# Performance work log

Measured on AMD Instinct MI355X. Metric: run time of the kernel, lower is better.

The kernel has to match this reference:

```python
import jax, jax.numpy as jnp
import numpy as np

DIM, E, K = 256, 8, 2
B, D, H, W = 1, 32, 32, 32
EPS = 1e-5


def setup_inputs() -> dict:
    key = jax.random.key(0)
    ks = jax.random.split(key, 16)
    nrm = lambda k, s, sc=0.02: jax.random.normal(k, s, jnp.float32) * sc
    def resblock_params(k):
        k1, k2, k3, k4 = jax.random.split(k, 4)
        return dict(
            c1w=nrm(k1, (DIM, DIM, 3, 3, 3)), c1b=jnp.zeros((DIM,), jnp.float32),
            g1=jax.random.uniform(k2, (DIM,), jnp.float32, 0.5, 1.5), be1=jnp.zeros((DIM,), jnp.float32),
            c2w=nrm(k3, (DIM, DIM, 3, 3, 3)), c2b=jnp.zeros((DIM,), jnp.float32),
            g2=jax.random.uniform(k4, (DIM,), jnp.float32, 0.5, 1.5), be2=jnp.zeros((DIM,), jnp.float32),
        )
    p1 = resblock_params(ks[5])
    p2 = resblock_params(ks[6])
    return {
        "x": jax.random.normal(ks[0], (B, DIM, D, H, W), jnp.float32),
        "wg": nrm(ks[1], (DIM, E)),
        "w1": nrm(ks[2], (E, DIM, DIM)), "b1": jnp.zeros((E, DIM), jnp.float32),
        "w2": nrm(ks[3], (E, DIM, DIM)), "b2": jnp.zeros((E, DIM), jnp.float32),
        "r1_c1w": p1["c1w"], "r1_c1b": p1["c1b"], "r1_g1": p1["g1"], "r1_be1": p1["be1"],
        "r1_c2w": p1["c2w"], "r1_c2b": p1["c2b"], "r1_g2": p1["g2"], "r1_be2": p1["be2"],
        "r2_c1w": p2["c1w"], "r2_c1b": p2["c1b"], "r2_g1": p2["g1"], "r2_be1": p2["be1"],
        "r2_c2w": p2["c2w"], "r2_c2b": p2["c2b"], "r2_g2": p2["g2"], "r2_be2": p2["be2"],
        "c8w": nrm(ks[4], (DIM, DIM, 1, 1, 1)), "c8b": jnp.zeros((DIM,), jnp.float32),
    }


def conv3d(x, w, b, pad):
    y = jax.lax.conv_general_dilated(
        x, w, window_strides=(1, 1, 1), padding=[(pad, pad)] * 3,
        dimension_numbers=("NCDHW", "OIDHW", "NCDHW"))
    return y + b[None, :, None, None, None]


def batchnorm(x, g, b):
    m = x.mean(axis=(0, 2, 3, 4), keepdims=True)
    v = x.var(axis=(0, 2, 3, 4), keepdims=True)
    return g[None, :, None, None, None] * (x - m) * jax.lax.rsqrt(v + EPS) + b[None, :, None, None, None]


def unet_res_block(x, c1w, c1b, g1, be1, c2w, c2b, g2, be2):
    out = jax.nn.leaky_relu(batchnorm(conv3d(x, c1w, c1b, 1), g1, be1), 0.01)
    out = batchnorm(conv3d(out, c2w, c2b, 1), g2, be2)
    return jax.nn.leaky_relu(out + x, 0.01)  # identity shortcut (in==out ch, stride 1)


def mom_block(x, wg, w1, b1, w2, b2):
    Bb, C, Dd, Hh, Ww = x.shape
    tokens = x.transpose(0, 2, 3, 4, 1).reshape(-1, C)  # [T, C]
    T = tokens.shape[0]
    probs = jax.nn.softmax(tokens @ wg, axis=-1)          # [T, E]
    vals, idx = jax.lax.top_k(probs, K)                   # [T, K]
    wts = vals / vals.sum(-1, keepdims=True)
    gates = jnp.zeros((T, E), probs.dtype).at[jnp.arange(T)[:, None], idx].set(wts)
    # dense expert MLPs (math-equivalent to gather/dispatch/combine)
    h = jax.nn.gelu(jnp.einsum("tc,ech->eth", tokens, w1) + b1[:, None, :])
    eo = jnp.einsum("eth,ehc->etc", h, w2) + b2[:, None, :]
    moe = jnp.einsum("te,etc->tc", gates, eo)             # [T, C]
    # switch-style load-balancing auxiliary loss
    density = (gates > 0).astype(probs.dtype).mean(0)     # fraction of tokens per expert
    density_proxy = probs.mean(0)
    aux = (density * density_proxy).sum() * E
    out = x + moe.reshape(Bb, Dd, Hh, Ww, C).transpose(0, 4, 1, 2, 3)
    return out, aux


def reference(x, wg, w1, b1, w2, b2,
              r1_c1w, r1_c1b, r1_g1, r1_be1, r1_c2w, r1_c2b, r1_g2, r1_be2,
              r2_c1w, r2_c1b, r2_g1, r2_be1, r2_c2w, r2_c2b, r2_g2, r2_be2,
              c8w, c8b):
    xm, aux = mom_block(x, wg, w1, b1, w2, b2)
    res = unet_res_block(xm, r1_c1w, r1_c1b, r1_g1, r1_be1, r1_c2w, r1_c2b, r1_g2, r1_be2)
    res = unet_res_block(res, r2_c1w, r2_c1b, r2_g1, r2_be1, r2_c2w, r2_c2b, r2_g2, r2_be2)
    out = xm + conv3d(res, c8w, c8b, 0)  # Dropout3d is identity at eval
    return out, aux
```

## Files before the change

kernel.cpp:

```cpp
#include <hip/hip_runtime.h>
#include <stdint.h>

typedef __attribute__((ext_vector_type(8))) short short8;
typedef __attribute__((ext_vector_type(4))) float f32x4;
typedef unsigned short u16;
typedef unsigned int u32;
typedef unsigned long long u64;

#define WS_TOK   0ull
#define WS_XT    16777216ull
#define WS_XMCT  50331648ull
#define WS_GATES 83886080ull
#define WS_PART  84934656ull
#define WS_MOE   101711872ull
#define WS_P1    135266304ull
#define WS_P2    155389952ull
#define WS_Y     175513600ull
#define WS_R2    209068032ull
#define WS_WRB   225845248ull
#define WS_W1P   240001024ull
#define WS_W2P   241049600ull
#define WS_C8P   242098176ull
#define WS_SF    242753536ull
#define WS_AUXP  242755584ull

__device__ __forceinline__ u16 f2bf(float f) {
  u32 x = __float_as_uint(f);
  u32 r = x + 0x7fffu + ((x >> 16) & 1u);
  return (u16)(r >> 16);
}

__global__ void trans_in_k(const float* __restrict__ x, float* __restrict__ xt,
                           u16* __restrict__ tok) {
  __shared__ float ld[64][65];
  int tt = blockIdx.x, cc = blockIdx.y, tid = threadIdx.x;
#pragma unroll
  for (int k = 0; k < 16; ++k) {
    int idx = tid + k * 256;
    int cl = idx >> 6, j = idx & 63;
    ld[cl][j] = x[(size_t)(cc * 64 + cl) * 32768 + tt * 64 + j];
  }
  __syncthreads();
#pragma unroll
  for (int k = 0; k < 16; ++k) {
    int idx = tid + k * 256;
    int tl = idx >> 6, cl = idx & 63;
    float v = ld[cl][tl];
    size_t o = (size_t)(tt * 64 + tl) * 256 + cc * 64 + cl;
    xt[o] = v;
    tok[o] = f2bf(v);
  }
}

__global__ void pack_rb_k(const float* __restrict__ w0, const float* __restrict__ w1,
                          const float* __restrict__ w2, const float* __restrict__ w3,
                          u16* __restrict__ out) {
  __shared__ float ld[6912];
  int conv = blockIdx.x >> 8, blk = blockIdx.x & 255, tid = threadIdx.x;
  const float* src = conv == 0 ? w0 : conv == 1 ? w1 : conv == 2 ? w2 : w3;
  size_t base = (size_t)blk * 256 * 27;
#pragma unroll
  for (int k = 0; k < 27; ++k) ld[tid + k * 256] = src[base + tid + k * 256];
  __syncthreads();
  u16* dst = out + (size_t)conv * 27 * 65536;
  int n = blk * 256 + tid;
#pragma unroll
  for (int tap = 0; tap < 27; ++tap)
    dst[(size_t)tap * 65536 + n] = f2bf(ld[tid * 27 + tap]);
}

__global__ void pack_tr_k(const float* __restrict__ w1, const float* __restrict__ w2,
                          u16* __restrict__ w1p, u16* __restrict__ w2p) {
  __shared__ float ld[64][65];
  int m = blockIdx.y, tile = blockIdx.x, tid = threadIdx.x;
  const float* src = (m < 8) ? (w1 + (size_t)m * 65536) : (w2 + (size_t)(m - 8) * 65536);
  u16* dst = (m < 8) ? (w1p + (size_t)m * 65536) : (w2p + (size_t)(m - 8) * 65536);
  int r0 = (tile >> 2) * 64, c0 = (tile & 3) * 64;
#pragma unroll
  for (int k = 0; k < 16; ++k) {
    int idx = tid + k * 256;
    int rr = idx >> 6, cc = idx & 63;
    ld[rr][cc] = src[(size_t)(r0 + rr) * 256 + c0 + cc];
  }
  __syncthreads();
#pragma unroll
  for (int k = 0; k < 16; ++k) {
    int idx = tid + k * 256;
    int cc = idx >> 6, rr = idx & 63;
    dst[(size_t)(c0 + cc) * 256 + r0 + rr] = f2bf(ld[rr][cc]);
  }
}

__global__ void cvt_k(const float* __restrict__ in, u16* __restrict__ out, int n) {
  int i = blockIdx.x * 256 + threadIdx.x;
  if (i < n) out[i] = f2bf(in[i]);
}

__global__ void halo_k(u16* __restrict__ P1, u16* __restrict__ P2) {
  int gid = blockIdx.x * 256 + threadIdx.x;
  int r = gid >> 5, o = (gid & 31) << 3;
  if (r >= 39304) return;
  int d = r / 1156, rem = r - d * 1156, h = rem / 34, w = rem - h * 34;
  if (d >= 1 && d <= 32 && h >= 1 && h <= 32 && w >= 1 && w <= 32) return;
  uint4 z = {0u, 0u, 0u, 0u};
  *(uint4*)(P1 + (size_t)r * 256 + o) = z;
  *(uint4*)(P2 + (size_t)r * 256 + o) = z;
}

__global__ void gate_k(const float* __restrict__ xt, const float* __restrict__ wg,
                       float* __restrict__ gates, float* __restrict__ auxp) {
  __shared__ float wgs[2048];
  __shared__ float ax[4][16];
  int tid = threadIdx.x;
#pragma unroll
  for (int k = 0; k < 8; ++k) wgs[tid + k * 256] = wg[tid + k * 256];
  __syncthreads();
  int t = blockIdx.x * 256 + tid;
  int lane = tid & 63, wv = tid >> 6;
  float l[8] = {0, 0, 0, 0, 0, 0, 0, 0};
  const float* xr = xt + (size_t)t * 256;
  for (int c = 0; c < 256; c += 4) {
    float4 xv = *(const float4*)(xr + c);
#pragma unroll
    for (int e = 0; e < 8; ++e)
      l[e] += xv.x * wgs[c * 8 + e] + xv.y * wgs[(c + 1) * 8 + e] +
              xv.z * wgs[(c + 2) * 8 + e] + xv.w * wgs[(c + 3) * 8 + e];
  }
  float mx = l[0];
#pragma unroll
  for (int e = 1; e < 8; ++e) mx = fmaxf(mx, l[e]);
  float p[8], sum = 0.f;
#pragma unroll
  for (int e = 0; e < 8; ++e) { p[e] = __expf(l[e] - mx); sum += p[e]; }
  float inv = 1.0f / sum;
#pragma unroll
  for (int e = 0; e < 8; ++e) p[e] *= inv;
  int i0 = 0; float v0 = p[0];
#pragma unroll
  for (int e = 1; e < 8; ++e) if (p[e] > v0) { v0 = p[e]; i0 = e; }
  int i1 = -1; float v1 = -1.0f;
#pragma unroll
  for (int e = 0; e < 8; ++e) if (e != i0 && p[e] > v1) { v1 = p[e]; i1 = e; }
  float wsum = v0 + v1;
  float g0 = v0 / wsum, g1 = v1 / wsum;
  float* gr = gates + (size_t)t * 8;
#pragma unroll
  for (int e = 0; e < 8; ++e) gr[e] = (e == i0) ? g0 : (e == i1) ? g1 : 0.0f;
#pragma unroll
  for (int e = 0; e < 8; ++e) {
    float ps = p[e];
    float cn = (e == i0 || e == i1) ? 1.0f : 0.0f;
    for (int o = 32; o; o >>= 1) { ps += __shfl_down(ps, o); cn += __shfl_down(cn, o); }
    if (lane == 0) { ax[wv][e] = ps; ax[wv][8 + e] = cn; }
  }
  __syncthreads();
  if (tid < 16)
    auxp[blockIdx.x * 16 + tid] = ax[0][tid] + ax[1][tid] + ax[2][tid] + ax[3][tid];
}

__global__ void aux_k(const float* __restrict__ auxp, float* __restrict__ out) {
  __shared__ float s[16];
  int i = threadIdx.x;
  if (i < 16) {
    float a = 0;
    for (int b = 0; b < 128; ++b) a += auxp[b * 16 + i];
    s[i] = a;
  }
  __syncthreads();
  if (i == 0) {
    float r = 0;
    for (int e = 0; e < 8; ++e)
      r += (s[8 + e] * (1.0f / 32768.0f)) * (s[e] * (1.0f / 32768.0f));
    out[0] = r * 8.0f;
  }
}

__global__ __launch_bounds__(512, 2) void moe_k(
    const u16* __restrict__ tok, const u16* __restrict__ w1p,
    const u16* __restrict__ w2p, const float* __restrict__ b1,
    const float* __restrict__ b2, const float* __restrict__ gates,
    float* __restrict__ moe) {
  __shared__ __attribute__((aligned(16))) unsigned char smem[163840];
  const int tid = threadIdx.x;
  const int ttile = blockIdx.x;
  const int lane = tid & 63;
  const int wv = tid >> 6;
  const int wr = (wv >> 2) * 64;
  const int wc = (wv & 3) * 64;
  const int fq = lane >> 4, fr = lane & 15;

#pragma unroll
  for (int it = 0; it < 8; ++it) {
    int s = tid + it * 512;
    int r = s >> 5, seg = s & 31;
    int cole = ((seg >> 3) << 6) + (((seg & 7) ^ (r & 7)) << 3);
    __builtin_amdgcn_global_load_lds(
        (const __attribute__((address_space(1))) u32*)(tok + (size_t)(ttile * 128 + r) * 256 + cole),
        (__attribute__((address_space(3))) u32*)(smem + s * 16), 16, 0, 0);
  }

  f32x4 macc[4][4];
#pragma unroll
  for (int m = 0; m < 4; ++m)
#pragma unroll
    for (int n = 0; n < 4; ++n) macc[m][n] = (f32x4){0.f, 0.f, 0.f, 0.f};

#pragma unroll 1
  for (int e = 0; e < 8; ++e) {
    const u16* w1e = w1p + e * 65536;
    const u16* w2e = w2p + e * 65536;

    f32x4 acc1[4][4];
#pragma unroll
    for (int mc = 0; mc < 4; ++mc)
#pragma unroll
      for (int nt = 0; nt < 4; ++nt) acc1[mc][nt] = (f32x4){0.f, 0.f, 0.f, 0.f};

#pragma unroll 1
    for (int kc = 0; kc < 4; ++kc) {
#pragma unroll
      for (int it = 0; it < 4; ++it) {
        int s = tid + it * 512;
        int r = s >> 3;
        int sub = (s & 7) ^ (r & 7);
        __builtin_amdgcn_global_load_lds(
            (const __attribute__((address_space(1))) u32*)(w1e + (size_t)r * 256 + kc * 64 + sub * 8),
            (__attribute__((address_space(3))) u32*)(smem + 65536 + s * 16), 16, 0, 0);
      }
      __syncthreads();
#pragma unroll
      for (int khf = 0; khf < 2; ++khf) {
        short8 af1[4], bt[4];
#pragma unroll
        for (int mc = 0; mc < 4; ++mc) {
          int row = wc + mc * 16 + fr;
          int p = (khf * 4 + fq) ^ (row & 7);
          af1[mc] = *(const short8*)(smem + 65536 + row * 128 + p * 16);
        }
#pragma unroll
        for (int nt = 0; nt < 4; ++nt) {
          int row = wr + nt * 16 + fr;
          int p = (khf * 4 + fq) ^ (row & 7);
          bt[nt] = *(const short8*)(smem + row * 512 + kc * 128 + p * 16);
        }
#pragma unroll
        for (int mc = 0; mc < 4; ++mc)
#pragma unroll
          for (int nt = 0; nt < 4; ++nt)
            acc1[mc][nt] = __builtin_amdgcn_mfma_f32_16x16x32_bf16(af1[mc], bt[nt], acc1[mc][nt], 0, 0, 0);
      }
      __syncthreads();
    }

#pragma unroll
    for (int mc = 0; mc < 4; ++mc) {
      int k0 = wc + mc * 16 + fq * 4;
      float4 bv = *(const float4*)(b1 + e * 256 + k0);
#pragma unroll
      for (int nt = 0; nt < 4; ++nt) {
        int t = wr + nt * 16 + fr;
        u64 pk = 0;
#pragma unroll
        for (int j = 0; j < 4; ++j) {
          float v = acc1[mc][nt][j] + ((const float*)&bv)[j];
          float u = 1.5957691216057308f * (v + 0.044715f * v * v * v);
          float g = v / (1.0f + __expf(-u));
          pk |= (u64)f2bf(g) << (16 * j);
        }
        *(u64*)(smem + 98304 + t * 512 + ((k0 * 2) ^ ((t & 7) << 4))) = pk;
      }
    }

    f32x4 acc2[4][4];
#pragma unroll
    for (int m = 0; m < 4; ++m)
#pragma unroll
      for (int n = 0; n < 4; ++n) acc2[m][n] = (f32x4){0.f, 0.f, 0.f, 0.f};

#pragma unroll 1
    for (int kc = 0; kc < 4; ++kc) {
#pragma unroll
      for (int it = 0; it < 4; ++it) {
        int s = tid + it * 512;
        int r = s >> 3;
        int sub = (s & 7) ^ (r & 7);
        __builtin_amdgcn_global_load_lds(
            (const __attribute__((address_space(1))) u32*)(w2e + (size_t)r * 256 + kc * 64 + sub * 8),
            (__attribute__((address_space(3))) u32*)(smem + 65536 + s * 16), 16, 0, 0);
      }
      __syncthreads();
#pragma unroll
      for (int khf = 0; khf < 2; ++khf) {
        short8 af[4], bb[4];
#pragma unroll
        for (int m = 0; m < 4; ++m) {
          int row = wr + m * 16 + fr;
          int col = (kc * 128 + (khf * 4 + fq) * 16) ^ ((row & 7) << 4);
          af[m] = *(const short8*)(smem + 98304 + row * 512 + col);
        }
#pragma unroll
        for (int n = 0; n < 4; ++n) {
          int row = wc + n * 16 + fr;
          int p = (khf * 4 + fq) ^ (row & 7);
          bb[n] = *(const short8*)(smem + 65536 + row * 128 + p * 16);
        }
#pragma unroll
        for (int m = 0; m < 4; ++m)
#pragma unroll
          for (int n = 0; n < 4; ++n)
            acc2[m][n] = __builtin_amdgcn_mfma_f32_16x16x32_bf16(af[m], bb[n], acc2[m][n], 0, 0, 0);
      }
      __syncthreads();
    }

    float bs2[4];
#pragma unroll
    for (int n = 0; n < 4; ++n) bs2[n] = b2[e * 256 + wc + n * 16 + fr];
#pragma unroll
    for (int m = 0; m < 4; ++m)
#pragma unroll
      for (int j = 0; j < 4; ++j) {
        int t = ttile * 128 + wr + m * 16 + fq * 4 + j;
        float g = gates[(size_t)t * 8 + e];
#pragma unroll
        for (int n = 0; n < 4; ++n)
          macc[m][n][j] += g * (acc2[m][n][j] + bs2[n]);
      }
  }

#pragma unroll
  for (int m = 0; m < 4; ++m)
#pragma unroll
    for (int j = 0; j < 4; ++j) {
      int t = ttile * 128 + wr + m * 16 + fq * 4 + j;
      float* mr = moe + (size_t)t * 256 + wc;
#pragma unroll
      for (int n = 0; n < 4; ++n) mr[n * 16 + fr] = macc[m][n][j];
    }
}

template <int MODE>
__global__ __launch_bounds__(256, 2) void gemm_k(
    const u16* __restrict__ A, const u16* __restrict__ Bw,
    const float* __restrict__ bias, float* __restrict__ outF,
    const float* __restrict__ xmct, float* __restrict__ part) {
  __shared__ __attribute__((aligned(16))) unsigned char smem[32768];
  const int tid = threadIdx.x;
  const int ttile = blockIdx.x;
  const int ctile = blockIdx.y;
  const int lane = tid & 63;
  const int wv = tid >> 6;
  const int wr = (wv >> 1) << 6;
  const int wc = (wv & 1) << 6;
  const int fq = lane >> 4;
  const int fr = lane & 15;

  int aoff[4], boff[4];
#pragma unroll
  for (int it = 0; it < 4; ++it) {
    int s = tid + it * 256;
    int r = s >> 3;
    int lsg = (s & 7) ^ (r & 7);
    if (MODE == 0) {
      int dd = ttile >> 3;
      int h0 = (ttile & 7) << 2;
      int base = dd * 1156 + (h0 + (r >> 5)) * 34 + (r & 31);
      aoff[it] = base * 256 + lsg * 8;
    } else {
      aoff[it] = (ttile * 128 + r) * 256 + lsg * 8;
    }
    boff[it] = (ctile * 128 + r) * 256 + lsg * 8;
  }

  f32x4 acc[4][4];
#pragma unroll
  for (int m = 0; m < 4; ++m)
#pragma unroll
    for (int n = 0; n < 4; ++n) acc[m][n] = (f32x4){0.f, 0.f, 0.f, 0.f};

  const int nTap = (MODE == 0) ? 27 : 1;
#pragma unroll 1
  for (int tap = 0; tap < nTap; ++tap) {
    int atap = 0, btap = 0;
    if (MODE == 0) {
      atap = ((tap / 9) * 1156 + ((tap / 3) % 3) * 34 + (tap % 3)) * 256;
      btap = tap * 65536;
    }
#pragma unroll 1
    for (int kc = 0; kc < 4; ++kc) {
      const u16* Ak = A + atap + kc * 64;
      const u16* Bk = Bw + btap + kc * 64;
#pragma unroll
      for (int it = 0; it < 4; ++it) {
        __builtin_amdgcn_global_load_lds(
            (const __attribute__((address_space(1))) u32*)(Ak + aoff[it]),
            (__attribute__((address_space(3))) u32*)(smem + (tid + it * 256) * 16),
            16, 0, 0);
        __builtin_amdgcn_global_load_lds(
            (const __attribute__((address_space(1))) u32*)(Bk + boff[it]),
            (__attribute__((address_space(3))) u32*)(smem + 16384 + (tid + it * 256) * 16),
            16, 0, 0);
      }
      __syncthreads();
#pragma unroll
      for (int khf = 0; khf < 2; ++khf) {
        short8 af[4], bb[4];
#pragma unroll
        for (int m = 0; m < 4; ++m) {
          int row = wr + m * 16 + fr;
          int p = (khf * 4 + fq) ^ (row & 7);
          af[m] = *(const short8*)(smem + row * 128 + p * 16);
        }
#pragma unroll
        for (int n = 0; n < 4; ++n) {
          int row = wc + n * 16 + fr;
          int p = (khf * 4 + fq) ^ (row & 7);
          bb[n] = *(const short8*)(smem + 16384 + row * 128 + p * 16);
        }
#pragma unroll
        for (int m = 0; m < 4; ++m)
#pragma unroll
          for (int n = 0; n < 4; ++n)
            acc[m][n] = __builtin_amdgcn_mfma_f32_16x16x32_bf16(af[m], bb[n], acc[m][n], 0, 0, 0);
      }
      __syncthreads();
    }
  }

  float bs[4];
#pragma unroll
  for (int n = 0; n < 4; ++n) bs[n] = bias[ctile * 128 + wc + n * 16 + fr];

  if (MODE == 3) {
#pragma unroll
    for (int m = 0; m < 4; ++m) {
      int trow = ttile * 128 + wr + m * 16 + fq * 4;
#pragma unroll
      for (int n = 0; n < 4; ++n) {
        int oc = ctile * 128 + wc + n * 16 + fr;
        size_t o = (size_t)oc * 32768 + trow;
        float4 xv = *(const float4*)(xmct + o);
        float4 w;
        w.x = acc[m][n][0] + bs[n] + xv.x;
        w.y = acc[m][n][1] + bs[n] + xv.y;
        w.z = acc[m][n][2] + bs[n] + xv.z;
        w.w = acc[m][n][3] + bs[n] + xv.w;
        *(float4*)(outF + o) = w;
      }
    }
  } else {
    float sn[4] = {0, 0, 0, 0}, qn[4] = {0, 0, 0, 0};
#pragma unroll
    for (int m = 0; m < 4; ++m) {
#pragma unroll
      for (int j = 0; j < 4; ++j) {
        int t = ttile * 128 + wr + m * 16 + fq * 4 + j;
        float* yr = outF + (size_t)t * 256 + ctile * 128 + wc;
#pragma unroll
        for (int n = 0; n < 4; ++n) {
          float v = acc[m][n][j] + bs[n];
          yr[n * 16 + fr] = v;
          sn[n] += v;
          qn[n] += v * v;
        }
      }
    }
#pragma unroll
    for (int n = 0; n < 4; ++n) {
      float s = sn[n], q = qn[n];
      s += __shfl_xor(s, 16); s += __shfl_xor(s, 32);
      q += __shfl_xor(q, 16); q += __shfl_xor(q, 32);
      if (lane < 16) {
        int pi = (ttile * 2 + (wv >> 1)) * 256 + ctile * 128 + wc + n * 16 + fr;
        part[pi] = s;
        part[131072 + pi] = q;
      }
    }
  }
}

__global__ void stats2_k(const float* __restrict__ part, const float* __restrict__ g,
                         const float* __restrict__ be, float* __restrict__ sf) {
  __shared__ float sred[4][256], qred[4][256];
  int tid = threadIdx.x;
  int c = tid & 255, qd = tid >> 8;
  float s = 0, q = 0;
  for (int b = qd * 128; b < qd * 128 + 128; ++b) {
    s += part[b * 256 + c];
    q += part[131072 + b * 256 + c];
  }
  sred[qd][c] = s;
  qred[qd][c] = q;
  __syncthreads();
  if (qd == 0) {
    s = sred[0][c] + sred[1][c] + sred[2][c] + sred[3][c];
    q = qred[0][c] + qred[1][c] + qred[2][c] + qred[3][c];
    float mean = s * (1.0f / 32768.0f);
    float var = q * (1.0f / 32768.0f) - mean * mean;
    float a = g[c] * rsqrtf(var + 1e-5f);
    sf[c] = a;
    sf[256 + c] = be[c] - mean * a;
  }
}

template <int V>
__global__ void bn_k(const float* __restrict__ y, const float* __restrict__ sf,
                     const float* __restrict__ skip, u16* __restrict__ pad,
                     float* __restrict__ f32o, u16* __restrict__ bfo) {
  int gid = blockIdx.x * 256 + threadIdx.x;
  int t = gid >> 5, c0 = (gid & 31) << 3;
  size_t base = (size_t)t * 256 + c0;
  float v[8];
  const float4* yp = (const float4*)(y + base);
  float4 y0 = yp[0], y1 = yp[1];
  const float4* ap = (const float4*)(sf + c0);
  float4 a0 = ap[0], a1 = ap[1];
  const float4* shp = (const float4*)(sf + 256 + c0);
  float4 s0 = shp[0], s1 = shp[1];
  v[0] = a0.x * y0.x + s0.x; v[1] = a0.y * y0.y + s0.y;
  v[2] = a0.z * y0.z + s0.z; v[3] = a0.w * y0.w + s0.w;
  v[4] = a1.x * y1.x + s1.x; v[5] = a1.y * y1.y + s1.y;
  v[6] = a1.z * y1.z + s1.z; v[7] = a1.w * y1.w + s1.w;
  if (V >= 1) {
    const float4* kp = (const float4*)(skip + base);
    float4 k0 = kp[0], k1 = kp[1];
    v[0] += k0.x; v[1] += k0.y; v[2] += k0.z; v[3] += k0.w;
    v[4] += k1.x; v[5] += k1.y; v[6] += k1.z; v[7] += k1.w;
  }
#pragma unroll
  for (int i = 0; i < 8; ++i) v[i] = v[i] > 0.0f ? v[i] : 0.01f * v[i];
  if (V <= 1) {
    int d = t >> 10, h = (t >> 5) & 31, w = t & 31;
    int prow = (d + 1) * 1156 + (h + 1) * 34 + (w + 1);
    uint4 pk;
    pk.x = (u32)f2bf(v[0]) | ((u32)f2bf(v[1]) << 16);
    pk.y = (u32)f2bf(v[2]) | ((u32)f2bf(v[3]) << 16);
    pk.z = (u32)f2bf(v[4]) | ((u32)f2bf(v[5]) << 16);
    pk.w = (u32)f2bf(v[6]) | ((u32)f2bf(v[7]) << 16);
    *(uint4*)(pad + (size_t)prow * 256 + c0) = pk;
  }
  if (V == 1) {
    float4 o0 = {v[0], v[1], v[2], v[3]}, o1 = {v[4], v[5], v[6], v[7]};
    float4* fp = (float4*)(f32o + base);
    fp[0] = o0; fp[1] = o1;
  }
  if (V == 2) {
    uint4 pk;
    pk.x = (u32)f2bf(v[0]) | ((u32)f2bf(v[1]) << 16);
    pk.y = (u32)f2bf(v[2]) | ((u32)f2bf(v[3]) << 16);
    pk.z = (u32)f2bf(v[4]) | ((u32)f2bf(v[5]) << 16);
    pk.w = (u32)f2bf(v[6]) | ((u32)f2bf(v[7]) << 16);
    *(uint4*)(bfo + base) = pk;
  }
}

__global__ void xm_k(float* __restrict__ xt, const float* __restrict__ moe,
                     float* __restrict__ xmct, u16* __restrict__ pad) {
  __shared__ float ld[64][65];
  int tt = blockIdx.x, cc = blockIdx.y, tid = threadIdx.x;
#pragma unroll
  for (int k = 0; k < 16; ++k) {
    int idx = tid + k * 256;
    int tl = idx >> 6, cl = idx & 63;
    size_t o = (size_t)(tt * 64 + tl) * 256 + cc * 64 + cl;
    float v = xt[o] + moe[o];
    xt[o] = v;
    ld[tl][cl] = v;
    int t = tt * 64 + tl;
    int d = t >> 10, h = (t >> 5) & 31, w = t & 31;
    int prow = (d + 1) * 1156 + (h + 1) * 34 + (w + 1);
    pad[(size_t)prow * 256 + cc * 64 + cl] = f2bf(v);
  }
  __syncthreads();
#pragma unroll
  for (int k = 0; k < 16; ++k) {
    int idx = tid + k * 256;
    int cl = idx >> 6, tl = idx & 63;
    xmct[(size_t)(cc * 64 + cl) * 32768 + tt * 64 + tl] = ld[tl][cl];
  }
}

extern "C" void kernel_launch(void* const* d_in, const int* in_sizes, int n_in,
                              void* d_out, int out_size, void* d_ws, size_t ws_size,
                              hipStream_t stream) {
  (void)in_sizes; (void)n_in; (void)out_size; (void)ws_size;
  const float* x  = (const float*)d_in[0];
  const float* wg = (const float*)d_in[1];
  const float* w1 = (const float*)d_in[2];
  const float* b1 = (const float*)d_in[3];
  const float* w2 = (const float*)d_in[4];
  const float* b2 = (const float*)d_in[5];

  char* ws = (char*)d_ws;
  u16* tok    = (u16*)(ws + WS_TOK);
  float* xt   = (float*)(ws + WS_XT);
  float* xmct = (float*)(ws + WS_XMCT);
  float* gates= (float*)(ws + WS_GATES);
  float* part = (float*)(ws + WS_PART);
  float* moe  = (float*)(ws + WS_MOE);
  u16* P1     = (u16*)(ws + WS_P1);
  u16* P2     = (u16*)(ws + WS_P2);
  float* ybuf = (float*)(ws + WS_Y);
  u16* r2b    = (u16*)(ws + WS_R2);
  u16* wrb    = (u16*)(ws + WS_WRB);
  u16* w1p    = (u16*)(ws + WS_W1P);
  u16* w2p    = (u16*)(ws + WS_W2P);
  u16* c8p    = (u16*)(ws + WS_C8P);
  float* sf   = (float*)(ws + WS_SF);
  float* auxp = (float*)(ws + WS_AUXP);
  float* outp = (float*)d_out;

  halo_k<<<4913, 256, 0, stream>>>(P1, P2);
  trans_in_k<<<dim3(512, 4), 256, 0, stream>>>(x, xt, tok);
  pack_rb_k<<<1024, 256, 0, stream>>>((const float*)d_in[6], (const float*)d_in[10],
                                      (const float*)d_in[14], (const float*)d_in[18], wrb);
  pack_tr_k<<<dim3(16, 16), 256, 0, stream>>>(w1, w2, w1p, w2p);
  cvt_k<<<256, 256, 0, stream>>>((const float*)d_in[22], c8p, 65536);
  gate_k<<<128, 256, 0, stream>>>(xt, wg, gates, auxp);

  moe_k<<<256, 512, 0, stream>>>(tok, w1p, w2p, b1, b2, gates, moe);
  xm_k<<<dim3(512, 4), 256, 0, stream>>>(xt, moe, xmct, P1);

  gemm_k<0><<<dim3(256, 2), 256, 0, stream>>>(P1, wrb + 0 * 1769472, (const float*)d_in[7],
                                              ybuf, nullptr, part);
  stats2_k<<<1, 1024, 0, stream>>>(part, (const float*)d_in[8], (const float*)d_in[9], sf);
  bn_k<0><<<4096, 256, 0, stream>>>(ybuf, sf, nullptr, P2, nullptr, nullptr);
  gemm_k<0><<<dim3(256, 2), 256, 0, stream>>>(P2, wrb + 1 * 1769472, (const float*)d_in[11],
                                              ybuf, nullptr, part);
  stats2_k<<<1, 1024, 0, stream>>>(part, (const float*)d_in[12], (const float*)d_in[13], sf);
  bn_k<1><<<4096, 256, 0, stream>>>(ybuf, sf, xt, P1, xt, nullptr);

  gemm_k<0><<<dim3(256, 2), 256, 0, stream>>>(P1, wrb + 2 * 1769472, (const float*)d_in[15],
                                              ybuf, nullptr, part);
  stats2_k<<<1, 1024, 0, stream>>>(part, (const float*)d_in[16], (const float*)d_in[17], sf);
  bn_k<0><<<4096, 256, 0, stream>>>(ybuf, sf, nullptr, P2, nullptr, nullptr);
  gemm_k<0><<<dim3(256, 2), 256, 0, stream>>>(P2, wrb + 3 * 1769472, (const float*)d_in[19],
                                              ybuf, nullptr, part);
  stats2_k<<<1, 1024, 0, stream>>>(part, (const float*)d_in[20], (const float*)d_in[21], sf);
  bn_k<2><<<4096, 256, 0, stream>>>(ybuf, sf, xt, nullptr, nullptr, r2b);

  gemm_k<3><<<dim3(256, 2), 256, 0, stream>>>(r2b, c8p, (const float*)d_in[23], outp,
                                              xmct, nullptr);
  aux_k<<<1, 64, 0, stream>>>(auxp, outp + 8388608);
}
```

Before: 778.2 us.

## Replace dense MoE over all experts with sparse top-2 token dispatch

Instead of running every token through all 8 expert MLPs and weighting by gates, the gate kernel now records top-2 selections and per-block counts. A scan and scatter then build a per-expert permutation padded to 128-row tiles. A grouped GEMM kernel processes only routed tokens per expert tile and writes bf16 outputs, and a combine kernel gathers the two expert outputs per token. This cuts expert FLOPs roughly fourfold, at the cost of extra small launches, gathered loads and a bf16 rounding of expert outputs. The conv GEMM tile order is also swizzled for mode 0.

Result: faster. 718.3 us (-7.7%).

```diff
diff --git a/kernel.cpp b/kernel.cpp
--- a/kernel.cpp
+++ b/kernel.cpp
@@ -11,7 +11,7 @@
 #define WS_XT    16777216ull
 #define WS_XMCT  50331648ull
 #define WS_GATES 83886080ull
-#define WS_PART  84934656ull
+#define WS_H     84934656ull
 #define WS_MOE   101711872ull
 #define WS_P1    135266304ull
 #define WS_P2    155389952ull
@@ -21,8 +21,16 @@
 #define WS_W1P   240001024ull
 #define WS_W2P   241049600ull
 #define WS_C8P   242098176ull
-#define WS_SF    242753536ull
-#define WS_AUXP  242755584ull
+#define WS_PART  242229248ull
+#define WS_SF    243277824ull
+#define WS_AUXP  243279872ull
+
+#define WS_PERM  (WS_H + 0x00000ull)
+#define WS_TBL   (WS_H + 0x60000ull)
+#define WS_META  (WS_H + 0x70000ull)
+#define WS_BCNT  (WS_H + 0x80000ull)
+#define WS_BOFF  (WS_H + 0x90000ull)
+#define WS_SEL   (WS_H + 0x100000ull)
 
 __device__ __forceinline__ u16 f2bf(float f) {
   u32 x = __float_as_uint(f);
@@ -108,9 +116,11 @@
 }
 
 __global__ void gate_k(const float* __restrict__ xt, const float* __restrict__ wg,
-                       float* __restrict__ gates, float* __restrict__ auxp) {
+                       float* __restrict__ gw, u32* __restrict__ sel,
+                       u32* __restrict__ blk_cnt, float* __restrict__ auxp) {
   __shared__ float wgs[2048];
   __shared__ float ax[4][16];
+  __shared__ u32 bc[4][8];
   int tid = threadIdx.x;
 #pragma unroll
   for (int k = 0; k < 8; ++k) wgs[tid + k * 256] = wg[tid + k * 256];
@@ -142,10 +152,16 @@
 #pragma unroll
   for (int e = 0; e < 8; ++e) if (e != i0 && p[e] > v1) { v1 = p[e]; i1 = e; }
   float wsum = v0 + v1;
-  float g0 = v0 / wsum, g1 = v1 / wsum;
-  float* gr = gates + (size_t)t * 8;
-#pragma unroll
-  for (int e = 0; e < 8; ++e) gr[e] = (e == i0) ? g0 : (e == i1) ? g1 : 0.0f;
+  gw[t * 2] = v0 / wsum;
+  gw[t * 2 + 1] = v1 / wsum;
+  sel[t] = (u32)i0 | ((u32)i1 << 4);
+  u64 mm[8];
+#pragma unroll
+  for (int e = 0; e < 8; ++e) mm[e] = __ballot(i0 == e || i1 == e);
+  if (lane == 0) {
+#pragma unroll
+    for (int e = 0; e < 8; ++e) bc[wv][e] = (u32)__popcll(mm[e]);
+  }
 #pragma unroll
   for (int e = 0; e < 8; ++e) {
     float ps = p[e];
@@ -156,6 +172,8 @@
   __syncthreads();
   if (tid < 16)
     auxp[blockIdx.x * 16 + tid] = ax[0][tid] + ax[1][tid] + ax[2][tid] + ax[3][tid];
+  if (tid < 8)
+    blk_cnt[blockIdx.x * 8 + tid] = bc[0][tid] + bc[1][tid] + bc[2][tid] + bc[3][tid];
 }
 
 __global__ void aux_k(const float* __restrict__ auxp, float* __restrict__ out) {
@@ -175,168 +193,260 @@
   }
 }
 
-__global__ __launch_bounds__(512, 2) void moe_k(
-    const u16* __restrict__ tok, const u16* __restrict__ w1p,
-    const u16* __restrict__ w2p, const float* __restrict__ b1,
-    const float* __restrict__ b2, const float* __restrict__ gates,
-    float* __restrict__ moe) {
+__global__ void scan_k(const u32* __restrict__ blk_cnt, u32* __restrict__ blkoff,
+                       u32* __restrict__ tbl, u32* __restrict__ meta,
+                       u32* __restrict__ perm) {
+  __shared__ u32 tot[8], base[8], nck[8], cbase[8];
+  int tid = threadIdx.x;
+  if (tid < 8) {
+    u32 run = 0;
+    for (int b = 0; b < 128; ++b) {
+      blkoff[b * 8 + tid] = run;
+      run += blk_cnt[b * 8 + tid];
+    }
+    tot[tid] = run;
+  }
+  __syncthreads();
+  if (tid == 0) {
+    u32 acc = 0, c = 0;
+    for (int e = 0; e < 8; ++e) {
+      base[e] = acc;
+      u32 nc = (tot[e] + 127) >> 7;
+      nck[e] = nc;
+      cbase[e] = c;
+      acc += nc << 7;
+      c += nc;
+    }
+    meta[0] = c;
+  }
+  __syncthreads();
+  for (int i = tid; i < 1024; i += 256) blkoff[i] += base[i & 7];
+  if (tid < 8) {
+    for (u32 k = 0; k < nck[tid]; ++k)
+      tbl[cbase[tid] + k] = ((base[tid] + (k << 7)) << 4) | (u32)tid;
+    for (u32 sl = base[tid] + tot[tid]; sl < base[tid] + (nck[tid] << 7); ++sl)
+      perm[sl] = 0;
+  }
+}
+
+__global__ void scatter_k(const u32* __restrict__ sel, const u32* __restrict__ blkoff,
+                          u32* __restrict__ perm, u32* __restrict__ tpos) {
+  __shared__ u32 wcnt[4][8];
+  int tid = threadIdx.x, b = blockIdx.x;
+  int lane = tid & 63, wv = tid >> 6;
+  int t = b * 256 + tid;
+  u32 s = sel[t];
+  int i0 = s & 15, i1 = (s >> 4) & 15;
+  u64 mm[8];
+#pragma unroll
+  for (int e = 0; e < 8; ++e) mm[e] = __ballot(i0 == e || i1 == e);
+  if (lane == 0) {
+#pragma unroll
+    for (int e = 0; e < 8; ++e) wcnt[wv][e] = (u32)__popcll(mm[e]);
+  }
+  __syncthreads();
+  u64 lt = (1ull << lane) - 1ull;
+#pragma unroll
+  for (int e = 0; e < 8; ++e) {
+    bool is0 = (i0 == e), is1 = (i1 == e);
+    if (is0 || is1) {
+      u32 woff = 0;
+#pragma unroll
+      for (int w = 0; w < 4; ++w)
+        if (w < wv) woff += wcnt[w][e];
+      u32 pos = blkoff[b * 8 + e] + woff + (u32)__popcll(mm[e] & lt);
+      perm[pos] = (u32)t;
+      tpos[t * 2 + (is0 ? 0 : 1)] = pos;
+    }
+  }
+}
+
+__global__ __launch_bounds__(512, 2) void moe_gemm_k(
+    const u16* __restrict__ tok, const u32* __restrict__ perm,
+    const u32* __restrict__ tbl, const u32* __restrict__ meta,
+    const u16* __restrict__ w1p, const u16* __restrict__ w2p,
+    const float* __restrict__ b1, const float* __restrict__ b2,
+    u16* __restrict__ eo) {
   __shared__ __attribute__((aligned(16))) unsigned char smem[163840];
+  const int bid = blockIdx.x;
+  if ((u32)bid >= meta[0]) return;
+  const u32 ent = tbl[bid];
+  const int e = (int)(ent & 15u);
+  const int slot0 = (int)(ent >> 4);
   const int tid = threadIdx.x;
-  const int ttile = blockIdx.x;
   const int lane = tid & 63;
   const int wv = tid >> 6;
   const int wr = (wv >> 2) * 64;
   const int wc = (wv & 3) * 64;
   const int fq = lane >> 4, fr = lane & 15;
+  const u16* w1e = w1p + e * 65536;
+  const u16* w2e = w2p + e * 65536;
 
 #pragma unroll
   for (int it = 0; it < 8; ++it) {
     int s = tid + it * 512;
     int r = s >> 5, seg = s & 31;
     int cole = ((seg >> 3) << 6) + (((seg & 7) ^ (r & 7)) << 3);
+    u32 rowtok = perm[slot0 + r];
     __builtin_amdgcn_global_load_lds(
-        (const __attribute__((address_space(1))) u32*)(tok + (size_t)(ttile * 128 + r) * 256 + cole),
+        (const __attribute__((address_space(1))) u32*)(tok + (size_t)rowtok * 256 + cole),
         (__attribute__((address_space(3))) u32*)(smem + s * 16), 16, 0, 0);
   }
 
-  f32x4 macc[4][4];
+  f32x4 acc1[4][4];
+#pragma unroll
+  for (int mc = 0; mc < 4; ++mc)
+#pragma unroll
+    for (int nt = 0; nt < 4; ++nt) acc1[mc][nt] = (f32x4){0.f, 0.f, 0.f, 0.f};
+
+#pragma unroll 1
+  for (int kc = 0; kc < 4; ++kc) {
+#pragma unroll
+    for (int it = 0; it < 4; ++it) {
+      int s = tid + it * 512;
+      int r = s >> 3;
+      int sub = (s & 7) ^ (r & 7);
+      __builtin_amdgcn_global_load_lds(
+          (const __attribute__((address_space(1))) u32*)(w1e + (size_t)r * 256 + kc * 64 + sub * 8),
+          (__attribute__((address_space(3))) u32*)(smem + 65536 + s * 16), 16, 0, 0);
+    }
+    __syncthreads();
+#pragma unroll
+    for (int khf = 0; khf < 2; ++khf) {
+      short8 af1[4], bt[4];
+#pragma unroll
+      for (int mc = 0; mc < 4; ++mc) {
+        int row = wc + mc * 16 + fr;
+        int p = (khf * 4 + fq) ^ (row & 7);
+        af1[mc] = *(const short8*)(smem + 65536 + row * 128 + p * 16);
+      }
+#pragma unroll
+      for (int nt = 0; nt < 4; ++nt) {
+        int row = wr + nt * 16 + fr;
+        int p = (khf * 4 + fq) ^ (row & 7);
+        bt[nt] = *(const short8*)(smem + row * 512 + kc * 128 + p * 16);
+      }
+#pragma unroll
+      for (int mc = 0; mc < 4; ++mc)
+#pragma unroll
+        for (int nt = 0; nt < 4; ++nt)
+          acc1[mc][nt] = __builtin_amdgcn_mfma_f32_16x16x32_bf16(af1[mc], bt[nt], acc1[mc][nt], 0, 0, 0);
+    }
+    __syncthreads();
+  }
+
+#pragma unroll
+  for (int mc = 0; mc < 4; ++mc) {
+    int k0 = wc + mc * 16 + fq * 4;
+    float4 bv = *(const float4*)(b1 + e * 256 + k0);
+#pragma unroll
+    for (int nt = 0; nt < 4; ++nt) {
+      int t = wr + nt * 16 + fr;
+      u64 pk = 0;
+#pragma unroll
+      for (int j = 0; j < 4; ++j) {
+        float v = acc1[mc][nt][j] + ((const float*)&bv)[j];
+        float u = 1.5957691216057308f * (v + 0.044715f * v * v * v);
+        float g = v / (1.0f + __expf(-u));
+        pk |= (u64)f2bf(g) << (16 * j);
+      }
+      *(u64*)(smem + 98304 + t * 512 + ((k0 * 2) ^ ((t & 7) << 4))) = pk;
+    }
+  }
+
+  f32x4 acc2[4][4];
 #pragma unroll
   for (int m = 0; m < 4; ++m)
 #pragma unroll
-    for (int n = 0; n < 4; ++n) macc[m][n] = (f32x4){0.f, 0.f, 0.f, 0.f};
+    for (int n = 0; n < 4; ++n) acc2[m][n] = (f32x4){0.f, 0.f, 0.f, 0.f};
 
 #pragma unroll 1
-  for (int e = 0; e < 8; ++e) {
-    const u16* w1e = w1p + e * 65536;
-    const u16* w2e = w2p + e * 65536;
-
-    f32x4 acc1[4][4];
-#pragma unroll
-    for (int mc = 0; mc < 4; ++mc)
-#pragma unroll
-      for (int nt = 0; nt < 4; ++nt) acc1[mc][nt] = (f32x4){0.f, 0.f, 0.f, 0.f};
-
-#pragma unroll 1
-    for (int kc = 0; kc < 4; ++kc) {
-#pragma unroll
-      for (int it = 0; it < 4; ++it) {
-        int s = tid + it * 512;
-        int r = s >> 3;
-        int sub = (s & 7) ^ (r & 7);
-        __builtin_amdgcn_global_load_lds(
-            (const __attribute__((address_space(1))) u32*)(w1e + (size_t)r * 256 + kc * 64 + sub * 8),
-            (__attribute__((address_space(3))) u32*)(smem + 65536 + s * 16), 16, 0, 0);
-      }
-      __syncthreads();
-#pragma unroll
-      for (int khf = 0; khf < 2; ++khf) {
-        short8 af1[4], bt[4];
-#pragma unroll
-        for (int mc = 0; mc < 4; ++mc) {
-          int row = wc + mc * 16 + fr;
-          int p = (khf * 4 + fq) ^ (row & 7);
-          af1[mc] = *(const short8*)(smem + 65536 + row * 128 + p * 16);
-        }
-#pragma unroll
-        for (int nt = 0; nt < 4; ++nt) {
-          int row = wr + nt * 16 + fr;
-          int p = (khf * 4 + fq) ^ (row & 7);
-          bt[nt] = *(const short8*)(smem + row * 512 + kc * 128 + p * 16);
-        }
-#pragma unroll
-        for (int mc = 0; mc < 4; ++mc)
-#pragma unroll
-          for (int nt = 0; nt < 4; ++nt)
-            acc1[mc][nt] = __builtin_amdgcn_mfma_f32_16x16x32_bf16(af1[mc], bt[nt], acc1[mc][nt], 0, 0, 0);
-      }
-      __syncthreads();
-    }
-
-#pragma unroll
-    for (int mc = 0; mc < 4; ++mc) {
-      int k0 = wc + mc * 16 + fq * 4;
-      float4 bv = *(const float4*)(b1 + e * 256 + k0);
-#pragma unroll
-      for (int nt = 0; nt < 4; ++nt) {
-        int t = wr + nt * 16 + fr;
-        u64 pk = 0;
-#pragma unroll
-        for (int j = 0; j < 4; ++j) {
-          float v = acc1[mc][nt][j] + ((const float*)&bv)[j];
-          float u = 1.5957691216057308f * (v + 0.044715f * v * v * v);
-          float g = v / (1.0f + __expf(-u));
-          pk |= (u64)f2bf(g) << (16 * j);
-        }
-        *(u64*)(smem + 98304 + t * 512 + ((k0 * 2) ^ ((t & 7) << 4))) = pk;
-      }
-    }
-
-    f32x4 acc2[4][4];
-#pragma unroll
-    for (int m = 0; m < 4; ++m)
-#pragma unroll
-      for (int n = 0; n < 4; ++n) acc2[m][n] = (f32x4){0.f, 0.f, 0.f, 0.f};
-
-#pragma unroll 1
-    for (int kc = 0; kc < 4; ++kc) {
-#pragma unroll
-      for (int it = 0; it < 4; ++it) {
-        int s = tid + it * 512;
-        int r = s >> 3;
-        int sub = (s & 7) ^ (r & 7);
-        __builtin_amdgcn_global_load_lds(
-            (const __attribute__((address_space(1))) u32*)(w2e + (size_t)r * 256 + kc * 64 + sub * 8),
-            (__attribute__((address_space(3))) u32*)(smem + 65536 + s * 16), 16, 0, 0);
-      }
-      __syncthreads();
-#pragma unroll
-      for (int khf = 0; khf < 2; ++khf) {
-        short8 af[4], bb[4];
-#pragma unroll
-        for (int m = 0; m < 4; ++m) {
-          int row = wr + m * 16 + fr;
-          int col = (kc * 128 + (khf * 4 + fq) * 16) ^ ((row & 7) << 4);
-          af[m] = *(const short8*)(smem + 98304 + row * 512 + col);
-        }
-#pragma unroll
-        for (int n = 0; n < 4; ++n) {
-          int row = wc + n * 16 + fr;
-          int p = (khf * 4 + fq) ^ (row & 7);
-          bb[n] = *(const short8*)(smem + 65536 + row * 128 + p * 16);
-        }
-#pragma unroll
-        for (int m = 0; m < 4; ++m)
-#pragma unroll
-          for (int n = 0; n < 4; ++n)
-            acc2[m][n] = __builtin_amdgcn_mfma_f32_16x16x32_bf16(af[m], bb[n], acc2[m][n], 0, 0, 0);
-      }
-      __syncthreads();
-    }
-
-    float bs2[4];
-#pragma unroll
-    for (int n = 0; n < 4; ++n) bs2[n] = b2[e * 256 + wc + n * 16 + fr];
-#pragma unroll
-    for (int m = 0; m < 4; ++m)
-#pragma unroll
-      for (int j = 0; j < 4; ++j) {
-        int t = ttile * 128 + wr + m * 16 + fq * 4 + j;
-        float g = gates[(size_t)t * 8 + e];
+  for (int kc = 0; kc < 4; ++kc) {
+#pragma unroll
+    for (int it = 0; it < 4; ++it) {
+      int s = tid + it * 512;
+      int r = s >> 3;
+      int sub = (s & 7) ^ (r & 7);
+      __builtin_amdgcn_global_load_lds(
+          (const __attribute__((address_space(1))) u32*)(w2e + (size_t)r * 256 + kc * 64 + sub * 8),
+          (__attribute__((address_space(3))) u32*)(smem + 65536 + s * 16), 16, 0, 0);
+    }
+    __syncthreads();
+#pragma unroll
+    for (int khf = 0; khf < 2; ++khf) {
+      short8 af[4], bb[4];
+#pragma unroll
+      for (int m = 0; m < 4; ++m) {
+        int row = wr + m * 16 + fr;
+        int col = (kc * 128 + (khf * 4 + fq) * 16) ^ ((row & 7) << 4);
+        af[m] = *(const short8*)(smem + 98304 + row * 512 + col);
+      }
+#pragma unroll
+      for (int n = 0; n < 4; ++n) {
+        int row = wc + n * 16 + fr;
+        int p = (khf * 4 + fq) ^ (row & 7);
+        bb[n] = *(const short8*)(smem + 65536 + row * 128 + p * 16);
+      }
+#pragma unroll
+      for (int m = 0; m < 4; ++m)
 #pragma unroll
         for (int n = 0; n < 4; ++n)
-          macc[m][n][j] += g * (acc2[m][n][j] + bs2[n]);
-      }
-  }
-
+          acc2[m][n] = __builtin_amdgcn_mfma_f32_16x16x32_bf16(af[m], bb[n], acc2[m][n], 0, 0, 0);
+    }
+    __syncthreads();
+  }
+
+  float bs2[4];
+#pragma unroll
+  for (int n = 0; n < 4; ++n) bs2[n] = b2[e * 256 + wc + n * 16 + fr];
 #pragma unroll
   for (int m = 0; m < 4; ++m)
 #pragma unroll
     for (int j = 0; j < 4; ++j) {
-      int t = ttile * 128 + wr + m * 16 + fq * 4 + j;
-      float* mr = moe + (size_t)t * 256 + wc;
-#pragma unroll
-      for (int n = 0; n < 4; ++n) mr[n * 16 + fr] = macc[m][n][j];
-    }
+      int rowslot = slot0 + wr + m * 16 + fq * 4 + j;
+      u16* er = eo + (size_t)rowslot * 256 + wc;
+#pragma unroll
+      for (int n = 0; n < 4; ++n) er[n * 16 + fr] = f2bf(acc2[m][n][j] + bs2[n]);
+    }
+}
+
+__global__ void combine_k(float* __restrict__ xt, const u16* __restrict__ eo,
+                          const float* __restrict__ gw, const u32* __restrict__ tpos,
+                          float* __restrict__ xmct, u16* __restrict__ pad) {
+  __shared__ float ld[64][65];
+  __shared__ u32 pp[64][2];
+  __shared__ float gg[64][2];
+  int tt = blockIdx.x, cc = blockIdx.y, tid = threadIdx.x;
+  if (tid < 128) {
+    int tl = tid >> 1, s = tid & 1;
+    int t = tt * 64 + tl;
+    pp[tl][s] = tpos[t * 2 + s];
+    gg[tl][s] = gw[t * 2 + s];
+  }
+  __syncthreads();
+#pragma unroll
+  for (int k = 0; k < 16; ++k) {
+    int idx = tid + k * 256;
+    int tl = idx >> 6, cl = idx & 63;
+    int c = cc * 64 + cl;
+    size_t o = (size_t)(tt * 64 + tl) * 256 + c;
+    float e0 = __uint_as_float((u32)eo[(size_t)pp[tl][0] * 256 + c] << 16);
+    float e1 = __uint_as_float((u32)eo[(size_t)pp[tl][1] * 256 + c] << 16);
+    float v = xt[o] + gg[tl][0] * e0 + gg[tl][1] * e1;
+    xt[o] = v;
+    ld[tl][cl] = v;
+    int t = tt * 64 + tl;
+    int d = t >> 10, h = (t >> 5) & 31, w = t & 31;
+    int prow = (d + 1) * 1156 + (h + 1) * 34 + (w + 1);
+    pad[(size_t)prow * 256 + c] = f2bf(v);
+  }
+  __syncthreads();
+#pragma unroll
+  for (int k = 0; k < 16; ++k) {
+    int idx = tid + k * 256;
+    int cl = idx >> 6, tl = idx & 63;
+    xmct[(size_t)(cc * 64 + cl) * 32768 + tt * 64 + tl] = ld[tl][cl];
+  }
 }
 
 template <int MODE>
@@ -346,7 +456,8 @@
     const float* __restrict__ xmct, float* __restrict__ part) {
   __shared__ __attribute__((aligned(16))) unsigned char smem[32768];
   const int tid = threadIdx.x;
-  const int ttile = blockIdx.x;
+  const int bx = blockIdx.x;
+  const int ttile = (MODE == 0) ? ((bx & 7) * 32 + (bx >> 3)) : bx;
   const int ctile = blockIdx.y;
   const int lane = tid & 63;
   const int wv = tid >> 6;
@@ -554,32 +665,6 @@
   }
 }
 
-__global__ void xm_k(float* __restrict__ xt, const float* __restrict__ moe,
-                     float* __restrict__ xmct, u16* __restrict__ pad) {
-  __shared__ float ld[64][65];
-  int tt = blockIdx.x, cc = blockIdx.y, tid = threadIdx.x;
-#pragma unroll
-  for (int k = 0; k < 16; ++k) {
-    int idx = tid + k * 256;
-    int tl = idx >> 6, cl = idx & 63;
-    size_t o = (size_t)(tt * 64 + tl) * 256 + cc * 64 + cl;
-    float v = xt[o] + moe[o];
-    xt[o] = v;
-    ld[tl][cl] = v;
-    int t = tt * 64 + tl;
-    int d = t >> 10, h = (t >> 5) & 31, w = t & 31;
-    int prow = (d + 1) * 1156 + (h + 1) * 34 + (w + 1);
-    pad[(size_t)prow * 256 + cc * 64 + cl] = f2bf(v);
-  }
-  __syncthreads();
-#pragma unroll
-  for (int k = 0; k < 16; ++k) {
-    int idx = tid + k * 256;
-    int cl = idx >> 6, tl = idx & 63;
-    xmct[(size_t)(cc * 64 + cl) * 32768 + tt * 64 + tl] = ld[tl][cl];
-  }
-}
-
 extern "C" void kernel_launch(void* const* d_in, const int* in_sizes, int n_in,
                               void* d_out, int out_size, void* d_ws, size_t ws_size,
                               hipStream_t stream) {
@@ -595,17 +680,24 @@
   u16* tok    = (u16*)(ws + WS_TOK);
   float* xt   = (float*)(ws + WS_XT);
   float* xmct = (float*)(ws + WS_XMCT);
-  float* gates= (float*)(ws + WS_GATES);
-  float* part = (float*)(ws + WS_PART);
-  float* moe  = (float*)(ws + WS_MOE);
+  float* gw   = (float*)(ws + WS_GATES);
+  u32* tpos   = (u32*)(ws + WS_GATES + 0x80000ull);
+  u32* perm   = (u32*)(ws + WS_PERM);
+  u32* tbl    = (u32*)(ws + WS_TBL);
+  u32* meta   = (u32*)(ws + WS_META);
+  u32* bcnt   = (u32*)(ws + WS_BCNT);
+  u32* boff   = (u32*)(ws + WS_BOFF);
+  u32* selb   = (u32*)(ws + WS_SEL);
   u16* P1     = (u16*)(ws + WS_P1);
   u16* P2     = (u16*)(ws + WS_P2);
   float* ybuf = (float*)(ws + WS_Y);
+  u16* eo     = (u16*)(ws + WS_Y);
   u16* r2b    = (u16*)(ws + WS_R2);
   u16* wrb    = (u16*)(ws + WS_WRB);
   u16* w1p    = (u16*)(ws + WS_W1P);
   u16* w2p    = (u16*)(ws + WS_W2P);
   u16* c8p    = (u16*)(ws + WS_C8P);
+  float* part = (float*)(ws + WS_PART);
   float* sf   = (float*)(ws + WS_SF);
   float* auxp = (float*)(ws + WS_AUXP);
   float* outp = (float*)d_out;
@@ -616,10 +708,12 @@
                                       (const float*)d_in[14], (const float*)d_in[18], wrb);
   pack_tr_k<<<dim3(16, 16), 256, 0, stream>>>(w1, w2, w1p, w2p);
   cvt_k<<<256, 256, 0, stream>>>((const float*)d_in[22], c8p, 65536);
-  gate_k<<<128, 256, 0, stream>>>(xt, wg, gates, auxp);
-
-  moe_k<<<256, 512, 0, stream>>>(tok, w1p, w2p, b1, b2, gates, moe);
-  xm_k<<<dim3(512, 4), 256, 0, stream>>>(xt, moe, xmct, P1);
+
+  gate_k<<<128, 256, 0, stream>>>(xt, wg, gw, selb, bcnt, auxp);
+  scan_k<<<1, 256, 0, stream>>>(bcnt, boff, tbl, meta, perm);
+  scatter_k<<<128, 256, 0, stream>>>(selb, boff, perm, tpos);
+  moe_gemm_k<<<520, 512, 0, stream>>>(tok, perm, tbl, meta, w1p, w2p, b1, b2, eo);
+  combine_k<<<dim3(512, 4), 256, 0, stream>>>(xt, eo, gw, tpos, xmct, P1);
 
   gemm_k<0><<<dim3(256, 2), 256, 0, stream>>>(P1, wrb + 0 * 1769472, (const float*)d_in[7],
                                               ybuf, nullptr, part);
```
